# Kernel tuning notes

Measured on AMD Instinct MI355X. Metric: run time of the kernel, lower is better.

Reference implementation:

```python
import jax, jax.numpy as jnp
import numpy as np
import math

V, D, H, L, F, S, B = 32000, 1024, 16, 6, 4096, 1024, 2
HD = D // H
EPS = 1e-5


def _pos_encoding(seq_len, d_model):
    pos = np.arange(seq_len, dtype=np.float32)[:, None]
    div = np.exp(np.arange(0, d_model, 2, dtype=np.float32) * (-math.log(10000.0) / d_model))
    pe = np.zeros((seq_len, d_model), dtype=np.float32)
    pe[:, 0::2] = np.sin(pos * div)
    pe[:, 1::2] = np.cos(pos * div)
    return jnp.asarray(pe)


def setup_inputs() -> dict:
    key = jax.random.key(0)
    ks = jax.random.split(key, 24)
    s = 0.02
    emb = jax.random.normal(ks[0], (V, D), jnp.float32) * s
    emb = emb.at[0].set(0.0)  # padding_idx=0
    return {
        "input_ids": jax.random.randint(ks[1], (B, S), 0, V),
        "emb": emb,
        "Wq": jax.random.normal(ks[2], (L, D, D), jnp.float32) * s,
        "bq": jnp.zeros((L, D), jnp.float32),
        "Wk": jax.random.normal(ks[3], (L, D, D), jnp.float32) * s,
        "bk": jnp.zeros((L, D), jnp.float32),
        "Wv": jax.random.normal(ks[4], (L, D, D), jnp.float32) * s,
        "bv": jnp.zeros((L, D), jnp.float32),
        "Wo": jax.random.normal(ks[5], (L, D, D), jnp.float32) * s,
        "bo": jnp.zeros((L, D), jnp.float32),
        "ln1_g": jnp.ones((L, D), jnp.float32),
        "ln1_b": jnp.zeros((L, D), jnp.float32),
        "ln2_g": jnp.ones((L, D), jnp.float32),
        "ln2_b": jnp.zeros((L, D), jnp.float32),
        "W1": jax.random.normal(ks[6], (L, D, F), jnp.float32) * s,
        "b1": jnp.zeros((L, F), jnp.float32),
        "W2": jax.random.normal(ks[7], (L, F, D), jnp.float32) * s,
        "b2": jnp.zeros((L, D), jnp.float32),
        "fn_g": jnp.ones((D,), jnp.float32),
        "fn_b": jnp.zeros((D,), jnp.float32),
        "Wout": jax.random.normal(ks[8], (D, V), jnp.float32) * s,
        "bout": jnp.zeros((V,), jnp.float32),
    }


def _layernorm(x, g, b):
    m = jnp.mean(x, axis=-1, keepdims=True)
    v = jnp.mean(jnp.square(x - m), axis=-1, keepdims=True)
    return (x - m) * jax.lax.rsqrt(v + EPS) * g + b


def reference(input_ids, emb, Wq, bq, Wk, bk, Wv, bv, Wo, bo,
              ln1_g, ln1_b, ln2_g, ln2_b, W1, b1, W2, b2,
              fn_g, fn_b, Wout, bout):
    b, s = input_ids.shape
    x = emb[input_ids] * math.sqrt(D)          # [B,S,D]
    x = x + _pos_encoding(s, D)[None]           # positional encoding (dropout off: eval)
    causal = jnp.tril(jnp.ones((s, s), dtype=bool))  # True where allowed
    for i in range(L):
        h = _layernorm(x, ln1_g[i], ln1_b[i])
        q = (h @ Wq[i] + bq[i]).reshape(b, s, H, HD).transpose(0, 2, 1, 3)
        k = (h @ Wk[i] + bk[i]).reshape(b, s, H, HD).transpose(0, 2, 1, 3)
        v = (h @ Wv[i] + bv[i]).reshape(b, s, H, HD).transpose(0, 2, 1, 3)
        scores = jnp.einsum('bhqd,bhkd->bhqk', q, k) / math.sqrt(HD)
        scores = jnp.where(causal, scores, -jnp.inf)
        attn = jax.nn.softmax(scores, axis=-1)
        ctx = jnp.einsum('bhqk,bhkd->bhqd', attn, v)
        ctx = ctx.transpose(0, 2, 1, 3).reshape(b, s, D)
        x = x + (ctx @ Wo[i] + bo[i])
        h2 = _layernorm(x, ln2_g[i], ln2_b[i])
        ff = jax.nn.gelu(h2 @ W1[i] + b1[i], approximate=False) @ W2[i] + b2[i]
        x = x + ff
    x = _layernorm(x, fn_g, fn_b)
    logits = x @ Wout + bout                   # [B,S,V]
    return logits
```

## Files before the change

kernel.cpp:

```cpp
#include <hip/hip_runtime.h>
#include <math.h>

#define V_   32000
#define D_   1024
#define H_   16
#define HD_  64
#define L_   6
#define F_   4096
#define S_   1024
#define B_   2
#define MTOK (B_*S_)
#define EPSLN 1e-5f

typedef unsigned short ushort_t;
typedef __attribute__((ext_vector_type(8))) short  s16x8;
typedef __attribute__((ext_vector_type(4))) float  f32x4;
typedef __attribute__((ext_vector_type(4))) unsigned short u16x4;

__device__ __forceinline__ float bf2f(unsigned short u) {
    unsigned int x = ((unsigned int)u) << 16;
    return __builtin_bit_cast(float, x);
}
__device__ __forceinline__ unsigned short f2bf(float f) {
    unsigned int x = __builtin_bit_cast(unsigned int, f);
    unsigned int r = (x + 0x7FFFu + ((x >> 16) & 1u)) >> 16;
    return (unsigned short)r;
}
__device__ __forceinline__ float gelu_f(float x) {
    float y = 0.7978845608f * (x + 0.044715f * x * x * x);
    float t = 1.0f - 2.0f / (__expf(2.0f * y) + 1.0f);
    return 0.5f * x * (1.0f + t);
}

__device__ __forceinline__ float blk_sum(float v, float* sb) {
    #pragma unroll
    for (int o = 32; o; o >>= 1) v += __shfl_xor(v, o, 64);
    int w = threadIdx.x >> 6;
    __syncthreads();
    if ((threadIdx.x & 63) == 0) sb[w] = v;
    __syncthreads();
    return sb[0] + sb[1] + sb[2] + sb[3];
}

template<bool GELU, bool OUTBF>
__global__ __launch_bounds__(512, 2)
void gemm256(const ushort_t* __restrict__ A, int lda,
             const ushort_t* __restrict__ BT, int ldb,
             void* __restrict__ Cv, int ldc,
             const float* __restrict__ bias,
             int M, int N, int K)
{
    int nmt = M >> 8;
    int nwg = gridDim.x * gridDim.y;
    int id  = blockIdx.x + gridDim.x * blockIdx.y;
    int swz = ((nwg & 7) == 0) ? ((id & 7) * (nwg >> 3) + (id >> 3)) : id;
    int m0 = (swz % nmt) << 8;
    int n0 = (swz / nmt) << 8;

    __shared__ __align__(16) ushort_t lA[2][256 * 64];
    __shared__ __align__(16) ushort_t lB[2][256 * 64];

    int tid  = threadIdx.x;
    int lane = tid & 63, wave = tid >> 6;
    int lr = lane & 15, lg = lane >> 4;
    int wm = wave >> 2, wn = wave & 3;

    f32x4 acc[8][4] = {};
    int nkt = K >> 6;

    auto stageu = [&](int buf, int kt, int sel) {
        int k0 = kt << 6;
        const ushort_t* src = (sel < 2) ? A : BT;
        int ld    = (sel < 2) ? lda : ldb;
        int rbase = ((sel < 2) ? m0 : n0) + ((sel & 1) << 7);
        ushort_t* dst = ((sel < 2) ? &lA[buf][0] : &lB[buf][0]) + ((sel & 1) << 13);
        #pragma unroll
        for (int r = 0; r < 2; ++r) {
            int e8  = r * 512 + tid;
            int row = e8 >> 3, slot = e8 & 7;
            int ls  = slot ^ (row & 7);
            const ushort_t* g = src + (size_t)(rbase + row) * ld + k0 + ls * 8;
            __builtin_amdgcn_global_load_lds(
                (const __attribute__((address_space(1))) void*)g,
                (__attribute__((address_space(3))) void*)(dst + e8 * 8), 16, 0, 0);
        }
    };
    auto rdA = [&](int buf, int row, int ks) -> s16x8 {
        int sl = (lg + ks * 4) ^ (row & 7);
        return *(const s16x8*)&lA[buf][row * 64 + sl * 8];
    };
    auto rdB = [&](int buf, int row, int ks) -> s16x8 {
        int sl = (lg + ks * 4) ^ (row & 7);
        return *(const s16x8*)&lB[buf][row * 64 + sl * 8];
    };

    stageu(0, 0, 0); stageu(0, 0, 1); stageu(0, 0, 2); stageu(0, 0, 3);
    if (nkt > 1) {
        stageu(1, 1, 2); stageu(1, 1, 3);
        asm volatile("s_waitcnt vmcnt(4)" ::: "memory");
    } else {
        asm volatile("s_waitcnt vmcnt(0)" ::: "memory");
    }
    __builtin_amdgcn_sched_barrier(0);
    __builtin_amdgcn_s_barrier();

    for (int u = 0; u < nkt; ++u) {
        int cur = u & 1, nxt = cur ^ 1;
        s16x8 af0[4][2], af1[4][2], bf0[2][2], bf1[2][2];

        #pragma unroll
        for (int mf = 0; mf < 4; ++mf)
            #pragma unroll
            for (int ks = 0; ks < 2; ++ks)
                af0[mf][ks] = rdA(cur, wm * 128 + mf * 16 + lr, ks);
        #pragma unroll
        for (int nf = 0; nf < 2; ++nf)
            #pragma unroll
            for (int ks = 0; ks < 2; ++ks) {
                bf0[nf][ks] = rdB(cur, wn * 64 + nf * 16 + lr, ks);
                bf1[nf][ks] = rdB(cur, wn * 64 + 32 + nf * 16 + lr, ks);
            }
        if (u + 1 < nkt) { stageu(nxt, u + 1, 0); stageu(nxt, u + 1, 1); }
        __builtin_amdgcn_s_barrier();
        asm volatile("s_waitcnt lgkmcnt(0)" ::: "memory");
        __builtin_amdgcn_sched_barrier(0);
        __builtin_amdgcn_s_setprio(1);
        #pragma unroll
        for (int mf = 0; mf < 4; ++mf)
            #pragma unroll
            for (int ks = 0; ks < 2; ++ks) {
                #pragma unroll
                for (int nf = 0; nf < 2; ++nf) {
                    acc[mf][nf]     = __builtin_amdgcn_mfma_f32_16x16x32_bf16(
                        af0[mf][ks], bf0[nf][ks], acc[mf][nf], 0, 0, 0);
                    acc[mf][2 + nf] = __builtin_amdgcn_mfma_f32_16x16x32_bf16(
                        af0[mf][ks], bf1[nf][ks], acc[mf][2 + nf], 0, 0, 0);
                }
            }
        __builtin_amdgcn_s_setprio(0);
        __builtin_amdgcn_s_barrier();

        #pragma unroll
        for (int mf = 0; mf < 4; ++mf)
            #pragma unroll
            for (int ks = 0; ks < 2; ++ks)
                af1[mf][ks] = rdA(cur, wm * 128 + 64 + mf * 16 + lr, ks);
        if (u + 2 < nkt) { stageu(cur, u + 2, 2); stageu(cur, u + 2, 3); }
        __builtin_amdgcn_s_barrier();
        asm volatile("s_waitcnt lgkmcnt(0)" ::: "memory");
        __builtin_amdgcn_sched_barrier(0);
        __builtin_amdgcn_s_setprio(1);
        #pragma unroll
        for (int mf = 0; mf < 4; ++mf)
            #pragma unroll
            for (int ks = 0; ks < 2; ++ks) {
                #pragma unroll
                for (int nf = 0; nf < 2; ++nf) {
                    acc[4 + mf][nf]     = __builtin_amdgcn_mfma_f32_16x16x32_bf16(
                        af1[mf][ks], bf0[nf][ks], acc[4 + mf][nf], 0, 0, 0);
                    acc[4 + mf][2 + nf] = __builtin_amdgcn_mfma_f32_16x16x32_bf16(
                        af1[mf][ks], bf1[nf][ks], acc[4 + mf][2 + nf], 0, 0, 0);
                }
            }
        __builtin_amdgcn_s_setprio(0);
        if (u + 2 < nkt) asm volatile("s_waitcnt vmcnt(4)" ::: "memory");
        else             asm volatile("s_waitcnt vmcnt(0)" ::: "memory");
        __builtin_amdgcn_sched_barrier(0);
        __builtin_amdgcn_s_barrier();
    }

    float*    Cf = (float*)Cv;
    ushort_t* Cb = (ushort_t*)Cv;
    #pragma unroll
    for (int mf = 0; mf < 8; ++mf) {
        int gm0 = m0 + wm * 128 + mf * 16 + lg * 4;
        #pragma unroll
        for (int nf = 0; nf < 4; ++nf) {
            int gn = n0 + wn * 64 + nf * 16 + lr;
            float bv = bias ? bias[gn] : 0.f;
            #pragma unroll
            for (int j = 0; j < 4; ++j) {
                float v = acc[mf][nf][j] + bv;
                if (GELU) v = gelu_f(v);
                size_t ci = (size_t)(gm0 + j) * ldc + gn;
                if (OUTBF) Cb[ci] = f2bf(v);
                else       Cf[ci] = v;
            }
        }
    }
}

template<int BN, bool GELU, bool RES, bool OUTBF, bool VOUT>
__global__ __launch_bounds__(256)
void gemm_bt(const ushort_t* __restrict__ A, int lda,
             const ushort_t* __restrict__ BT, int ldb,
             void* __restrict__ Cv, int ldc,
             const float* __restrict__ bias,
             const float* __restrict__ res,
             int M, int N, int K, ushort_t* __restrict__ vtp)
{
    const int BK = 32;
    const int NF = BN / 32;
    int m0 = blockIdx.x * 128;
    int n0 = blockIdx.y * BN;

    __shared__ __align__(16) ushort_t lA[2][128 * BK];
    __shared__ __align__(16) ushort_t lB[2][BN * BK];

    int tid  = threadIdx.x;
    int lane = tid & 63;
    int wave = tid >> 6;
    int lr = lane & 15, lg = lane >> 4;
    int wr = wave >> 1, wc = wave & 1;

    f32x4 acc[4][NF] = {};
    int nkt = K / BK;

    auto stage = [&](int buf, int kt) {
        int k0 = kt * BK;
        #pragma unroll
        for (int i = 0; i < 2; ++i) {
            int e8  = i * 256 + tid;
            int row = e8 >> 2, slot = e8 & 3;
            int ls  = slot ^ (row & 3);
            const ushort_t* g = A + (size_t)(m0 + row) * lda + k0 + ls * 8;
            __builtin_amdgcn_global_load_lds(
                (const __attribute__((address_space(1))) void*)g,
                (__attribute__((address_space(3))) void*)&lA[buf][e8 * 8], 16, 0, 0);
        }
        #pragma unroll
        for (int i = 0; i < BN / 64; ++i) {
            int e8  = i * 256 + tid;
            int row = e8 >> 2, slot = e8 & 3;
            int ls  = slot ^ (row & 3);
            const ushort_t* g = BT + (size_t)(n0 + row) * ldb + k0 + ls * 8;
            __builtin_amdgcn_global_load_lds(
                (const __attribute__((address_space(1))) void*)g,
                (__attribute__((address_space(3))) void*)&lB[buf][e8 * 8], 16, 0, 0);
        }
    };

    stage(0, 0);
    __syncthreads();

    int cur = 0;
    for (int kt = 0; kt < nkt; ++kt) {
        if (kt + 1 < nkt) stage(cur ^ 1, kt + 1);
        __builtin_amdgcn_sched_barrier(0);
        s16x8 af[4], bfr[NF];
        #pragma unroll
        for (int m = 0; m < 4; ++m) {
            int row = wr * 64 + m * 16 + lr;
            int sl  = lg ^ (row & 3);
            af[m] = *(const s16x8*)&lA[cur][row * BK + sl * 8];
        }
        #pragma unroll
        for (int n = 0; n < NF; ++n) {
            int row = wc * (BN / 2) + n * 16 + lr;
            int sl  = lg ^ (row & 3);
            bfr[n] = *(const s16x8*)&lB[cur][row * BK + sl * 8];
        }
        #pragma unroll
        for (int m = 0; m < 4; ++m)
            #pragma unroll
            for (int n = 0; n < NF; ++n)
                acc[m][n] = __builtin_amdgcn_mfma_f32_16x16x32_bf16(
                    af[m], bfr[n], acc[m][n], 0, 0, 0);
        __syncthreads();
        cur ^= 1;
    }

    float*    Cf = (float*)Cv;
    ushort_t* Cb = (ushort_t*)Cv;
    #pragma unroll
    for (int m = 0; m < 4; ++m) {
        int gm0 = m0 + wr * 64 + m * 16 + lg * 4;
        #pragma unroll
        for (int n = 0; n < NF; ++n) {
            int gn = n0 + wc * (BN / 2) + n * 16 + lr;
            #pragma unroll
            for (int j = 0; j < 4; ++j) {
                float v = acc[m][n][j];
                if (bias) v += bias[gn];
                size_t ci = (size_t)(gm0 + j) * ldc + gn;
                if (RES)  v += res[ci];
                if (GELU) v = gelu_f(v);
                if (OUTBF) Cb[ci] = f2bf(v);
                else       Cf[ci] = v;
                if (VOUT && gn >= 2048) {
                    int hv = gn - 2048;
                    int mm = gm0 + j;
                    vtp[((size_t)(((mm >> 10) << 4) + (hv >> 6)) * 64
                         + (hv & 63)) * 1024 + (mm & 1023)] = f2bf(v);
                }
            }
        }
    }
}

__global__ __launch_bounds__(256)
void flash_attn(const ushort_t* __restrict__ qkv,
                const ushort_t* __restrict__ vt,
                ushort_t* __restrict__ ctx)
{
    const int QB = 64, KB = 64;
    int z  = blockIdx.y;
    int b  = z >> 4, hh = z & 15;

    __shared__ __align__(16) ushort_t Qs[QB * 64];
    __shared__ __align__(16) ushort_t Ks[2][KB * 64];
    __shared__ __align__(16) ushort_t Vs[2][64 * KB];
    __shared__ float    Ss[QB][68];
    __shared__ __align__(16) ushort_t Ps[QB][72];
    __shared__ float mrow[QB], lrow[QB], arow[QB];

    int tid  = threadIdx.x;
    int lane = tid & 63, wave = tid >> 6;
    int lr = lane & 15, lg = lane >> 4;
    int r = tid >> 2, p = tid & 3;

    auto stageKV = [&](int buf, int kv0) {
        const ushort_t* kbase = qkv + (size_t)(b * S_ + kv0) * 3072 + 1024 + hh * HD_;
        const ushort_t* vbase = vt + (size_t)z * HD_ * S_ + kv0;
        #pragma unroll
        for (int rnd = 0; rnd < 2; ++rnd) {
            int e8 = rnd * 256 + tid;
            int row = e8 >> 3, slot = e8 & 7;
            int ls = slot ^ (row & 7);
            const ushort_t* gk = kbase + (size_t)row * 3072 + ls * 8;
            __builtin_amdgcn_global_load_lds(
                (const __attribute__((address_space(1))) void*)gk,
                (__attribute__((address_space(3))) void*)&Ks[buf][e8 * 8], 16, 0, 0);
            const ushort_t* gv = vbase + (size_t)row * S_ + ls * 8;
            __builtin_amdgcn_global_load_lds(
                (const __attribute__((address_space(1))) void*)gv,
                (__attribute__((address_space(3))) void*)&Vs[buf][e8 * 8], 16, 0, 0);
        }
    };

    #pragma unroll
    for (int half = 0; half < 2; ++half) {
        int qt = half ? (15 - (int)blockIdx.x) : (int)blockIdx.x;
        int q0 = qt * QB;

        if (tid < QB) { mrow[tid] = -1e30f; lrow[tid] = 0.f; }
        const ushort_t* qbase = qkv + (size_t)(b * S_ + q0) * 3072 + hh * HD_;
        #pragma unroll
        for (int rnd = 0; rnd < 2; ++rnd) {
            int e8   = rnd * 256 + tid;
            int row  = e8 >> 3;
            int slot = e8 & 7;
            int ls   = slot ^ (row & 7);
            const ushort_t* g = qbase + (size_t)row * 3072 + ls * 8;
            __builtin_amdgcn_global_load_lds(
                (const __attribute__((address_space(1))) void*)g,
                (__attribute__((address_space(3))) void*)&Qs[e8 * 8], 16, 0, 0);
        }
        stageKV(0, 0);
        __syncthreads();

        s16x8 qa[4][2];
        #pragma unroll
        for (int mf = 0; mf < 4; ++mf)
            #pragma unroll
            for (int ks = 0; ks < 2; ++ks) {
                int row = mf * 16 + lr;
                int sl  = (lg + ks * 4) ^ (row & 7);
                qa[mf][ks] = *(const s16x8*)&Qs[row * 64 + sl * 8];
            }

        f32x4 acc[4] = {};
        int kv_end = q0 + QB;
        int cur = 0;
        for (int kv0 = 0; kv0 < kv_end; kv0 += KB) {
            if (kv0 + KB < kv_end) stageKV(cur ^ 1, kv0 + KB);

            s16x8 kb[2];
            #pragma unroll
            for (int ks = 0; ks < 2; ++ks) {
                int row = wave * 16 + lr;
                int sl  = (lg + ks * 4) ^ (row & 7);
                kb[ks] = *(const s16x8*)&Ks[cur][row * 64 + sl * 8];
            }
            f32x4 sa[4] = {};
            __builtin_amdgcn_s_setprio(1);
            #pragma unroll
            for (int mf = 0; mf < 4; ++mf)
                #pragma unroll
                for (int ks = 0; ks < 2; ++ks)
                    sa[mf] = __builtin_amdgcn_mfma_f32_16x16x32_bf16(
                        qa[mf][ks], kb[ks], sa[mf], 0, 0, 0);
            __builtin_amdgcn_s_setprio(0);

            int ki = kv0 + wave * 16 + lr;
            #pragma unroll
            for (int mf = 0; mf < 4; ++mf)
                #pragma unroll
                for (int j = 0; j < 4; ++j) {
                    int qi = q0 + mf * 16 + lg * 4 + j;
                    float s = (ki <= qi) ? sa[mf][j] * 0.125f : -1e30f;
                    Ss[mf * 16 + lg * 4 + j][wave * 16 + lr] = s;
                }
            __syncthreads();

            float mo = mrow[r];
            float sv[16];
            float pm = -1e30f;
            #pragma unroll
            for (int i = 0; i < 16; ++i) {
                sv[i] = Ss[r][p * 16 + i];
                pm = fmaxf(pm, sv[i]);
            }
            pm = fmaxf(pm, __shfl_xor(pm, 1, 64));
            pm = fmaxf(pm, __shfl_xor(pm, 2, 64));
            float M = fmaxf(mo, pm);
            float sum = 0.f;
            s16x8 pk0, pk1;
            #pragma unroll
            for (int i = 0; i < 8; ++i) {
                float e0 = __expf(sv[i] - M);
                float e1 = __expf(sv[i + 8] - M);
                sum += e0 + e1;
                pk0[i] = (short)f2bf(e0);
                pk1[i] = (short)f2bf(e1);
            }
            *(s16x8*)&Ps[r][p * 16]     = pk0;
            *(s16x8*)&Ps[r][p * 16 + 8] = pk1;
            sum += __shfl_xor(sum, 1, 64);
            sum += __shfl_xor(sum, 2, 64);
            if (p == 0) {
                float al = __expf(mo - M);
                arow[r] = al;
                mrow[r] = M;
                lrow[r] = lrow[r] * al + sum;
            }
            __syncthreads();

            #pragma unroll
            for (int mf = 0; mf < 4; ++mf) {
                #pragma unroll
                for (int j = 0; j < 4; ++j)
                    acc[mf][j] *= arow[mf * 16 + lg * 4 + j];
            }
            s16x8 vb[2];
            #pragma unroll
            for (int ks = 0; ks < 2; ++ks) {
                int row = wave * 16 + lr;
                int sl  = (lg + ks * 4) ^ (row & 7);
                vb[ks] = *(const s16x8*)&Vs[cur][row * 64 + sl * 8];
            }
            __builtin_amdgcn_s_setprio(1);
            #pragma unroll
            for (int mf = 0; mf < 4; ++mf)
                #pragma unroll
                for (int ks = 0; ks < 2; ++ks) {
                    s16x8 pa = *(const s16x8*)((const char*)&Ps[0][0]
                                + (mf * 16 + lr) * 144 + lg * 16 + ks * 64);
                    acc[mf] = __builtin_amdgcn_mfma_f32_16x16x32_bf16(
                        pa, vb[ks], acc[mf], 0, 0, 0);
                }
            __builtin_amdgcn_s_setprio(0);
            __syncthreads();
            cur ^= 1;
        }

        #pragma unroll
        for (int mf = 0; mf < 4; ++mf)
            #pragma unroll
            for (int j = 0; j < 4; ++j) {
                int rr = mf * 16 + lg * 4 + j;
                float o = acc[mf][j] / lrow[rr];
                ctx[(size_t)(b * S_ + q0 + rr) * D_ + hh * HD_ + wave * 16 + lr] = f2bf(o);
            }
        __syncthreads();
    }
}

__global__ __launch_bounds__(256)
void prep_layer(const float* __restrict__ Wq, const float* __restrict__ Wk,
                const float* __restrict__ Wv, const float* __restrict__ Wo,
                const float* __restrict__ W1, const float* __restrict__ W2,
                const float* __restrict__ bq, const float* __restrict__ bk,
                const float* __restrict__ bv,
                ushort_t* __restrict__ wqkvT, ushort_t* __restrict__ woT,
                ushort_t* __restrict__ w1T, ushort_t* __restrict__ w2T,
                float* __restrict__ qkvb)
{
    int bid = blockIdx.x;
    if (bid >= 3072) {
        int j = bid - 3072;
        const float* bsrc = (j == 0) ? bq : (j == 1) ? bk : bv;
        int c = threadIdx.x * 4;
        *(f32x4*)&qkvb[j * 1024 + c] = *(const f32x4*)&bsrc[c];
        return;
    }
    __shared__ float t[64][65];
    int tid = threadIdx.x;
    int tx = tid & 63, ty = tid >> 6;
    const float* src; ushort_t* dst; int R, C, c0, r0;
    if (bid < 1024) {
        int mat = bid >> 8, tnum = bid & 255;
        src = (mat == 0) ? Wq : (mat == 1) ? Wk : (mat == 2) ? Wv : Wo;
        dst = (mat < 3) ? (wqkvT + (size_t)mat * D_ * D_) : woT;
        R = D_; C = D_;
        c0 = (tnum & 15) * 64; r0 = (tnum >> 4) * 64;
    } else if (bid < 2048) {
        int tnum = bid - 1024;
        src = W1; dst = w1T; R = D_; C = F_;
        c0 = (tnum & 63) * 64; r0 = (tnum >> 6) * 64;
    } else {
        int tnum = bid - 2048;
        src = W2; dst = w2T; R = F_; C = D_;
        c0 = (tnum & 15) * 64; r0 = (tnum >> 4) * 64;
    }
    #pragma unroll
    for (int i = 0; i < 16; ++i)
        t[ty + i * 4][tx] = src[(size_t)(r0 + ty + i * 4) * C + c0 + tx];
    __syncthreads();
    int u = tid & 31, v = tid >> 5;
    #pragma unroll
    for (int i = 0; i < 8; ++i) {
        int cc = v + i * 8;
        unsigned int val = (unsigned int)f2bf(t[u * 2][cc])
                         | ((unsigned int)f2bf(t[u * 2 + 1][cc]) << 16);
        *(unsigned int*)&dst[(size_t)(c0 + cc) * R + r0 + u * 2] = val;
    }
}

__global__ __launch_bounds__(256)
void tconv(const float* __restrict__ in, ushort_t* __restrict__ out, int R, int C)
{
    __shared__ float t[64][65];
    int c0 = blockIdx.x * 64, r0 = blockIdx.y * 64;
    int tid = threadIdx.x;
    int tx = tid & 63, ty = tid >> 6;
    #pragma unroll
    for (int i = 0; i < 16; ++i)
        t[ty + i * 4][tx] = in[(size_t)(r0 + ty + i * 4) * C + c0 + tx];
    __syncthreads();
    int u = tid & 31, v = tid >> 5;
    #pragma unroll
    for (int i = 0; i < 8; ++i) {
        int cc = v + i * 8;
        unsigned int val = (unsigned int)f2bf(t[u * 2][cc])
                         | ((unsigned int)f2bf(t[u * 2 + 1][cc]) << 16);
        *(unsigned int*)&out[(size_t)(c0 + cc) * R + r0 + u * 2] = val;
    }
}

__global__ __launch_bounds__(256)
void embed_pe(const int* __restrict__ ids, const float* __restrict__ emb,
              float* __restrict__ x)
{
    int row = blockIdx.x;
    int s   = row & (S_ - 1);
    int id  = ids[row];
    int d   = threadIdx.x * 4;
    f32x4 ev = *(const f32x4*)&emb[(size_t)id * D_ + d];
    f32x4 o;
    #pragma unroll
    for (int j = 0; j < 4; ++j) {
        int dd = d + j;
        int i  = dd >> 1;
        float div = expf(-(float)(2 * i) * (9.210340371976184f / 1024.0f));
        float arg = (float)s * div;
        float pe  = (dd & 1) ? cosf(arg) : sinf(arg);
        o[j] = ev[j] * 32.0f + pe;
    }
    *(f32x4*)&x[(size_t)row * D_ + d] = o;
}

__global__ __launch_bounds__(256)
void ln_kernel(const float* __restrict__ x, const float* __restrict__ g,
               const float* __restrict__ b, ushort_t* __restrict__ out)
{
    __shared__ float sb[4];
    int row = blockIdx.x;
    const float* xr = x + (size_t)row * D_;
    int c = threadIdx.x * 4;
    f32x4 v = *(const f32x4*)&xr[c];
    float s = v[0] + v[1] + v[2] + v[3];
    s = blk_sum(s, sb);
    float mean = s * (1.0f / D_);
    f32x4 dv = v - mean;
    float sq = dv[0]*dv[0] + dv[1]*dv[1] + dv[2]*dv[2] + dv[3]*dv[3];
    sq = blk_sum(sq, sb);
    float rstd = rsqrtf(sq * (1.0f / D_) + EPSLN);
    u16x4 o;
    #pragma unroll
    for (int j = 0; j < 4; ++j)
        o[j] = f2bf(dv[j] * rstd * g[c + j] + b[c + j]);
    *(u16x4*)&out[(size_t)row * D_ + c] = o;
}

__global__ void ws_marker(float* o) { o[threadIdx.x] = -777777.0f; }

extern "C" void kernel_launch(void* const* d_in, const int* in_sizes, int n_in,
                              void* d_out, int out_size, void* d_ws, size_t ws_size,
                              hipStream_t stream)
{
    (void)in_sizes; (void)n_in; (void)out_size;
    const int*   ids  = (const int*)d_in[0];
    const float* emb  = (const float*)d_in[1];
    const float* Wq   = (const float*)d_in[2];
    const float* bq   = (const float*)d_in[3];
    const float* Wk   = (const float*)d_in[4];
    const float* bk   = (const float*)d_in[5];
    const float* Wv   = (const float*)d_in[6];
    const float* bv   = (const float*)d_in[7];
    const float* Wo   = (const float*)d_in[8];
    const float* bo   = (const float*)d_in[9];
    const float* ln1g = (const float*)d_in[10];
    const float* ln1b = (const float*)d_in[11];
    const float* ln2g = (const float*)d_in[12];
    const float* ln2b = (const float*)d_in[13];
    const float* W1   = (const float*)d_in[14];
    const float* b1   = (const float*)d_in[15];
    const float* W2   = (const float*)d_in[16];
    const float* b2   = (const float*)d_in[17];
    const float* fng  = (const float*)d_in[18];
    const float* fnb  = (const float*)d_in[19];
    const float* Wout = (const float*)d_in[20];
    const float* bout = (const float*)d_in[21];
    float* out = (float*)d_out;

    char* base = (char*)d_ws;
    size_t off = 0;
    float*    x    = (float*)(base + off);    off += (size_t)MTOK * D_ * 4;
    ushort_t* h    = (ushort_t*)(base + off); off += (size_t)MTOK * D_ * 2;
    ushort_t* qkv  = (ushort_t*)(base + off); off += (size_t)MTOK * 3 * D_ * 2;
    ushort_t* vt   = (ushort_t*)(base + off); off += (size_t)B_ * H_ * HD_ * S_ * 2;
    ushort_t* ctx  = (ushort_t*)(base + off); off += (size_t)MTOK * D_ * 2;
    ushort_t* ff   = (ushort_t*)(base + off); off += (size_t)MTOK * F_ * 2;
    float*    qkvb = (float*)(base + off);    off += 3072 * 4;
    ushort_t* wqkvT= (ushort_t*)(base + off); off += (size_t)3 * D_ * D_ * 2;
    ushort_t* woT  = (ushort_t*)(base + off); off += (size_t)D_ * D_ * 2;
    ushort_t* w1T  = (ushort_t*)(base + off); off += (size_t)D_ * F_ * 2;
    ushort_t* w2T  = (ushort_t*)(base + off); off += (size_t)F_ * D_ * 2;
    ushort_t* wouT = (ushort_t*)(base + off); off += (size_t)V_ * D_ * 2;
    if (ws_size < off) { ws_marker<<<1, 64, 0, stream>>>(out); return; }

    embed_pe<<<MTOK, 256, 0, stream>>>(ids, emb, x);

    for (int i = 0; i < L_; ++i) {
        prep_layer<<<3075, 256, 0, stream>>>(
            Wq + (size_t)i * D_ * D_, Wk + (size_t)i * D_ * D_,
            Wv + (size_t)i * D_ * D_, Wo + (size_t)i * D_ * D_,
            W1 + (size_t)i * D_ * F_, W2 + (size_t)i * F_ * D_,
            bq + i * D_, bk + i * D_, bv + i * D_,
            wqkvT, woT, w1T, w2T, qkvb);

        ln_kernel<<<MTOK, 256, 0, stream>>>(x, ln1g + i * D_, ln1b + i * D_, h);

        gemm_bt<128,false,false,true,true><<<dim3(16, 24), 256, 0, stream>>>(
            h, D_, wqkvT, D_, qkv, 3 * D_, qkvb, nullptr, MTOK, 3 * D_, D_, vt);

        flash_attn<<<dim3(8, B_ * H_), 256, 0, stream>>>(qkv, vt, ctx);

        gemm_bt<64,false,true,false,false><<<dim3(16, 16), 256, 0, stream>>>(
            ctx, D_, woT, D_, x, D_, bo + i * D_, x, MTOK, D_, D_, nullptr);

        ln_kernel<<<MTOK, 256, 0, stream>>>(x, ln2g + i * D_, ln2b + i * D_, h);

        gemm_bt<128,true,false,true,false><<<dim3(16, 32), 256, 0, stream>>>(
            h, D_, w1T, D_, ff, F_, b1 + i * F_, nullptr, MTOK, F_, D_, nullptr);

        gemm_bt<64,false,true,false,false><<<dim3(16, 16), 256, 0, stream>>>(
            ff, F_, w2T, F_, x, D_, b2 + i * D_, x, MTOK, D_, F_, nullptr);
    }

    ln_kernel<<<MTOK, 256, 0, stream>>>(x, fng, fnb, h);
    tconv<<<dim3(500, 16), 256, 0, stream>>>(Wout, wouT, D_, V_);
    gemm256<false,false><<<dim3(8, 125), 512, 0, stream>>>(
        h, D_, wouT, D_, out, V_, bout, MTOK, V_, D_);
}
```

Before: 1.582 ms.

## Deepen gemm_bt K-tile to 64 with swizzled grid; use it for output projection

The generic gemm_bt kernel now stages 64-wide K tiles with an 8-slot XOR swizzle, issues two MFMA k-steps per tile under raised wave priority, and remaps block IDs with an 8-way swizzle meant to improve L2 reuse. The specialised 256x256 gemm256 kernel for the final vocabulary projection is removed and replaced by gemm_bt with 128x128 tiles. This halves the barriers per K and aims for better cache locality. In exchange it doubles LDS use per block, which may reduce occupancy, and the logits GEMM loses the larger-tile, finer-pipelined kernel.

After: 1.562 ms. No clear change (-1.3%).

```diff
diff --git a/kernel.cpp b/kernel.cpp
--- a/kernel.cpp
+++ b/kernel.cpp
@@ -42,154 +42,6 @@
     return sb[0] + sb[1] + sb[2] + sb[3];
 }
 
-template<bool GELU, bool OUTBF>
-__global__ __launch_bounds__(512, 2)
-void gemm256(const ushort_t* __restrict__ A, int lda,
-             const ushort_t* __restrict__ BT, int ldb,
-             void* __restrict__ Cv, int ldc,
-             const float* __restrict__ bias,
-             int M, int N, int K)
-{
-    int nmt = M >> 8;
-    int nwg = gridDim.x * gridDim.y;
-    int id  = blockIdx.x + gridDim.x * blockIdx.y;
-    int swz = ((nwg & 7) == 0) ? ((id & 7) * (nwg >> 3) + (id >> 3)) : id;
-    int m0 = (swz % nmt) << 8;
-    int n0 = (swz / nmt) << 8;
-
-    __shared__ __align__(16) ushort_t lA[2][256 * 64];
-    __shared__ __align__(16) ushort_t lB[2][256 * 64];
-
-    int tid  = threadIdx.x;
-    int lane = tid & 63, wave = tid >> 6;
-    int lr = lane & 15, lg = lane >> 4;
-    int wm = wave >> 2, wn = wave & 3;
-
-    f32x4 acc[8][4] = {};
-    int nkt = K >> 6;
-
-    auto stageu = [&](int buf, int kt, int sel) {
-        int k0 = kt << 6;
-        const ushort_t* src = (sel < 2) ? A : BT;
-        int ld    = (sel < 2) ? lda : ldb;
-        int rbase = ((sel < 2) ? m0 : n0) + ((sel & 1) << 7);
-        ushort_t* dst = ((sel < 2) ? &lA[buf][0] : &lB[buf][0]) + ((sel & 1) << 13);
-        #pragma unroll
-        for (int r = 0; r < 2; ++r) {
-            int e8  = r * 512 + tid;
-            int row = e8 >> 3, slot = e8 & 7;
-            int ls  = slot ^ (row & 7);
-            const ushort_t* g = src + (size_t)(rbase + row) * ld + k0 + ls * 8;
-            __builtin_amdgcn_global_load_lds(
-                (const __attribute__((address_space(1))) void*)g,
-                (__attribute__((address_space(3))) void*)(dst + e8 * 8), 16, 0, 0);
-        }
-    };
-    auto rdA = [&](int buf, int row, int ks) -> s16x8 {
-        int sl = (lg + ks * 4) ^ (row & 7);
-        return *(const s16x8*)&lA[buf][row * 64 + sl * 8];
-    };
-    auto rdB = [&](int buf, int row, int ks) -> s16x8 {
-        int sl = (lg + ks * 4) ^ (row & 7);
-        return *(const s16x8*)&lB[buf][row * 64 + sl * 8];
-    };
-
-    stageu(0, 0, 0); stageu(0, 0, 1); stageu(0, 0, 2); stageu(0, 0, 3);
-    if (nkt > 1) {
-        stageu(1, 1, 2); stageu(1, 1, 3);
-        asm volatile("s_waitcnt vmcnt(4)" ::: "memory");
-    } else {
-        asm volatile("s_waitcnt vmcnt(0)" ::: "memory");
-    }
-    __builtin_amdgcn_sched_barrier(0);
-    __builtin_amdgcn_s_barrier();
-
-    for (int u = 0; u < nkt; ++u) {
-        int cur = u & 1, nxt = cur ^ 1;
-        s16x8 af0[4][2], af1[4][2], bf0[2][2], bf1[2][2];
-
-        #pragma unroll
-        for (int mf = 0; mf < 4; ++mf)
-            #pragma unroll
-            for (int ks = 0; ks < 2; ++ks)
-                af0[mf][ks] = rdA(cur, wm * 128 + mf * 16 + lr, ks);
-        #pragma unroll
-        for (int nf = 0; nf < 2; ++nf)
-            #pragma unroll
-            for (int ks = 0; ks < 2; ++ks) {
-                bf0[nf][ks] = rdB(cur, wn * 64 + nf * 16 + lr, ks);
-                bf1[nf][ks] = rdB(cur, wn * 64 + 32 + nf * 16 + lr, ks);
-            }
-        if (u + 1 < nkt) { stageu(nxt, u + 1, 0); stageu(nxt, u + 1, 1); }
-        __builtin_amdgcn_s_barrier();
-        asm volatile("s_waitcnt lgkmcnt(0)" ::: "memory");
-        __builtin_amdgcn_sched_barrier(0);
-        __builtin_amdgcn_s_setprio(1);
-        #pragma unroll
-        for (int mf = 0; mf < 4; ++mf)
-            #pragma unroll
-            for (int ks = 0; ks < 2; ++ks) {
-                #pragma unroll
-                for (int nf = 0; nf < 2; ++nf) {
-                    acc[mf][nf]     = __builtin_amdgcn_mfma_f32_16x16x32_bf16(
-                        af0[mf][ks], bf0[nf][ks], acc[mf][nf], 0, 0, 0);
-                    acc[mf][2 + nf] = __builtin_amdgcn_mfma_f32_16x16x32_bf16(
-                        af0[mf][ks], bf1[nf][ks], acc[mf][2 + nf], 0, 0, 0);
-                }
-            }
-        __builtin_amdgcn_s_setprio(0);
-        __builtin_amdgcn_s_barrier();
-
-        #pragma unroll
-        for (int mf = 0; mf < 4; ++mf)
-            #pragma unroll
-            for (int ks = 0; ks < 2; ++ks)
-                af1[mf][ks] = rdA(cur, wm * 128 + 64 + mf * 16 + lr, ks);
-        if (u + 2 < nkt) { stageu(cur, u + 2, 2); stageu(cur, u + 2, 3); }
-        __builtin_amdgcn_s_barrier();
-        asm volatile("s_waitcnt lgkmcnt(0)" ::: "memory");
-        __builtin_amdgcn_sched_barrier(0);
-        __builtin_amdgcn_s_setprio(1);
-        #pragma unroll
-        for (int mf = 0; mf < 4; ++mf)
-            #pragma unroll
-            for (int ks = 0; ks < 2; ++ks) {
-                #pragma unroll
-                for (int nf = 0; nf < 2; ++nf) {
-                    acc[4 + mf][nf]     = __builtin_amdgcn_mfma_f32_16x16x32_bf16(
-                        af1[mf][ks], bf0[nf][ks], acc[4 + mf][nf], 0, 0, 0);
-                    acc[4 + mf][2 + nf] = __builtin_amdgcn_mfma_f32_16x16x32_bf16(
-                        af1[mf][ks], bf1[nf][ks], acc[4 + mf][2 + nf], 0, 0, 0);
-                }
-            }
-        __builtin_amdgcn_s_setprio(0);
-        if (u + 2 < nkt) asm volatile("s_waitcnt vmcnt(4)" ::: "memory");
-        else             asm volatile("s_waitcnt vmcnt(0)" ::: "memory");
-        __builtin_amdgcn_sched_barrier(0);
-        __builtin_amdgcn_s_barrier();
-    }
-
-    float*    Cf = (float*)Cv;
-    ushort_t* Cb = (ushort_t*)Cv;
-    #pragma unroll
-    for (int mf = 0; mf < 8; ++mf) {
-        int gm0 = m0 + wm * 128 + mf * 16 + lg * 4;
-        #pragma unroll
-        for (int nf = 0; nf < 4; ++nf) {
-            int gn = n0 + wn * 64 + nf * 16 + lr;
-            float bv = bias ? bias[gn] : 0.f;
-            #pragma unroll
-            for (int j = 0; j < 4; ++j) {
-                float v = acc[mf][nf][j] + bv;
-                if (GELU) v = gelu_f(v);
-                size_t ci = (size_t)(gm0 + j) * ldc + gn;
-                if (OUTBF) Cb[ci] = f2bf(v);
-                else       Cf[ci] = v;
-            }
-        }
-    }
-}
-
 template<int BN, bool GELU, bool RES, bool OUTBF, bool VOUT>
 __global__ __launch_bounds__(256)
 void gemm_bt(const ushort_t* __restrict__ A, int lda,
@@ -199,10 +51,13 @@
              const float* __restrict__ res,
              int M, int N, int K, ushort_t* __restrict__ vtp)
 {
-    const int BK = 32;
+    const int BK = 64;
     const int NF = BN / 32;
-    int m0 = blockIdx.x * 128;
-    int n0 = blockIdx.y * BN;
+    int nwg = gridDim.x * gridDim.y;
+    int id  = blockIdx.x + gridDim.x * blockIdx.y;
+    int swz = ((nwg & 7) == 0) ? ((id & 7) * (nwg >> 3) + (id >> 3)) : id;
+    int m0 = (swz % gridDim.x) * 128;
+    int n0 = (swz / gridDim.x) * BN;
 
     __shared__ __align__(16) ushort_t lA[2][128 * BK];
     __shared__ __align__(16) ushort_t lB[2][BN * BK];
@@ -219,20 +74,20 @@
     auto stage = [&](int buf, int kt) {
         int k0 = kt * BK;
         #pragma unroll
-        for (int i = 0; i < 2; ++i) {
+        for (int i = 0; i < 4; ++i) {
             int e8  = i * 256 + tid;
-            int row = e8 >> 2, slot = e8 & 3;
-            int ls  = slot ^ (row & 3);
+            int row = e8 >> 3, slot = e8 & 7;
+            int ls  = slot ^ (row & 7);
             const ushort_t* g = A + (size_t)(m0 + row) * lda + k0 + ls * 8;
             __builtin_amdgcn_global_load_lds(
                 (const __attribute__((address_space(1))) void*)g,
                 (__attribute__((address_space(3))) void*)&lA[buf][e8 * 8], 16, 0, 0);
         }
         #pragma unroll
-        for (int i = 0; i < BN / 64; ++i) {
+        for (int i = 0; i < BN / 32; ++i) {
             int e8  = i * 256 + tid;
-            int row = e8 >> 2, slot = e8 & 3;
-            int ls  = slot ^ (row & 3);
+            int row = e8 >> 3, slot = e8 & 7;
+            int ls  = slot ^ (row & 7);
             const ushort_t* g = BT + (size_t)(n0 + row) * ldb + k0 + ls * 8;
             __builtin_amdgcn_global_load_lds(
                 (const __attribute__((address_space(1))) void*)g,
@@ -247,25 +102,35 @@
     for (int kt = 0; kt < nkt; ++kt) {
         if (kt + 1 < nkt) stage(cur ^ 1, kt + 1);
         __builtin_amdgcn_sched_barrier(0);
-        s16x8 af[4], bfr[NF];
+        s16x8 af[4][2], bfr[NF][2];
         #pragma unroll
         for (int m = 0; m < 4; ++m) {
             int row = wr * 64 + m * 16 + lr;
-            int sl  = lg ^ (row & 3);
-            af[m] = *(const s16x8*)&lA[cur][row * BK + sl * 8];
+            #pragma unroll
+            for (int ks = 0; ks < 2; ++ks) {
+                int sl = (lg + ks * 4) ^ (row & 7);
+                af[m][ks] = *(const s16x8*)&lA[cur][row * BK + sl * 8];
+            }
         }
         #pragma unroll
         for (int n = 0; n < NF; ++n) {
             int row = wc * (BN / 2) + n * 16 + lr;
-            int sl  = lg ^ (row & 3);
-            bfr[n] = *(const s16x8*)&lB[cur][row * BK + sl * 8];
-        }
+            #pragma unroll
+            for (int ks = 0; ks < 2; ++ks) {
+                int sl = (lg + ks * 4) ^ (row & 7);
+                bfr[n][ks] = *(const s16x8*)&lB[cur][row * BK + sl * 8];
+            }
+        }
+        __builtin_amdgcn_s_setprio(1);
         #pragma unroll
         for (int m = 0; m < 4; ++m)
             #pragma unroll
             for (int n = 0; n < NF; ++n)
-                acc[m][n] = __builtin_amdgcn_mfma_f32_16x16x32_bf16(
-                    af[m], bfr[n], acc[m][n], 0, 0, 0);
+                #pragma unroll
+                for (int ks = 0; ks < 2; ++ks)
+                    acc[m][n] = __builtin_amdgcn_mfma_f32_16x16x32_bf16(
+                        af[m][ks], bfr[n][ks], acc[m][n], 0, 0, 0);
+        __builtin_amdgcn_s_setprio(0);
         __syncthreads();
         cur ^= 1;
     }
@@ -671,6 +536,6 @@
 
     ln_kernel<<<MTOK, 256, 0, stream>>>(x, fng, fnb, h);
     tconv<<<dim3(500, 16), 256, 0, stream>>>(Wout, wouT, D_, V_);
-    gemm256<false,false><<<dim3(8, 125), 512, 0, stream>>>(
-        h, D_, wouT, D_, out, V_, bout, MTOK, V_, D_);
-}
+    gemm_bt<128,false,false,false,false><<<dim3(16, 250), 256, 0, stream>>>(
+        h, D_, wouT, D_, out, V_, bout, nullptr, MTOK, V_, D_, nullptr);
+}
```
